# Optimization experiments

Hardware: AMD Instinct MI355X
Metric: run time of the kernel (lower is better)

Reference implementation:

```python
import jax, jax.numpy as jnp
import numpy as np

ALPHA = 1.702
LIMIT = 7.0
TOP_K = 2
B, S, H, E, I = 2, 1024, 768, 8, 768


def setup_inputs() -> dict:
    key = jax.random.key(0)
    ks = jax.random.split(key, 7)
    scale = 0.02
    return {
        "hidden_states": jax.random.normal(ks[0], (B, S, H), dtype=jnp.float32),
        "Wr": jax.random.normal(ks[1], (H, E), dtype=jnp.float32) * scale,
        "br": jax.random.normal(ks[2], (E,), dtype=jnp.float32) * scale,
        "Wgu": jax.random.normal(ks[3], (E, H, 2 * I), dtype=jnp.float32) * scale,
        "bgu": jax.random.normal(ks[4], (E, 2 * I), dtype=jnp.float32) * scale,
        "Wd": jax.random.normal(ks[5], (E, I, H), dtype=jnp.float32) * scale,
        "bd": jax.random.normal(ks[6], (E, H), dtype=jnp.float32) * scale,
    }


def reference(hidden_states, Wr, br, Wgu, bgu, Wd, bd):
    # Router: top-K experts per token, softmax over the K selected logits
    logits = jnp.einsum("bsh,he->bse", hidden_states, Wr) + br
    topk_vals, topk_idx = jax.lax.top_k(logits, TOP_K)        # [B,S,K]
    router_scores = jax.nn.softmax(topk_vals, axis=-1)         # [B,S,K]

    # Dense-over-experts grouped GEMM (sparse_matmul reference: unselected
    # experts are computed but never read by the combine gather below).
    gu = jnp.einsum("bsh,ehf->bsef", hidden_states, Wgu) + bgu  # [B,S,E,2I]
    gu = jnp.minimum(gu, LIMIT)
    gate = gu[..., :I]
    up = jnp.maximum(gu[..., I:], -LIMIT)
    glu = gate * jax.nn.sigmoid(gate * ALPHA)
    activated = (up + 1.0) * glu                                # [B,S,E,I]

    down = jnp.einsum("bsei,eih->bseh", activated, Wd) + bd     # [B,S,E,H]

    # all_to_all_combine (num_devices=1): gather this token's K expert outputs
    sel = jnp.take_along_axis(down, topk_idx[..., None], axis=2)  # [B,S,K,H]
    output = jnp.sum(sel * router_scores[..., None], axis=2)      # [B,S,H]
    return output
```

## Files before the change

kernel.cpp:

```cpp
#include <hip/hip_runtime.h>
#include <hip/hip_bf16.h>
#include <cmath>

#define ALPHA 1.702f
#define LIMIT 7.0f

constexpr int B = 2, S = 1024, H = 768, E = 8, I = 768;
constexpr int T = B * S;
constexpr int TWO_I = 2 * I;
constexpr int CAP = T;
constexpr int NT1 = I / 64;
constexpr int NT2 = H / 64;
constexpr int MT = CAP / 128;

constexpr int RTR_BLKS = 64;
constexpr int WGU_TILES = E * (TWO_I / 64) * (H / 64);
constexpr int WD_TILES  = E * (H / 64) * (H / 64);
constexpr int PRE_BLKS = RTR_BLKS + WGU_TILES;
constexpr int G1_BLKS = MT * E * NT1;
constexpr int K1_BLKS = G1_BLKS + WD_TILES;
constexpr int G2_BLKS = MT * E * NT2;

typedef __attribute__((ext_vector_type(8))) short short8;
typedef __attribute__((ext_vector_type(4))) float floatx4;

__device__ __forceinline__ unsigned short f2bf(float v) {
  __hip_bfloat16 h = __float2bfloat16(v);
  return *reinterpret_cast<unsigned short*>(&h);
}

__device__ __forceinline__ void g2l16(const void* g, void* l) {
  __builtin_amdgcn_global_load_lds(
      (const __attribute__((address_space(1))) void*)g,
      (__attribute__((address_space(3))) void*)l, 16, 0, 0);
}

__device__ __forceinline__ void transpose_tile(
    const float* __restrict__ in, unsigned short* __restrict__ outw,
    int N, int n0, int k0, float (*tile)[65], int tid) {
  constexpr int K = 768;
  int jr = tid & 15, r0 = tid >> 4;
#pragma unroll
  for (int p = 0; p < 4; p++) {
    int k = r0 + p * 16;
    float4 v = *(const float4*)(in + (size_t)(k0 + k) * N + n0 + jr * 4);
    tile[k][jr * 4 + 0] = v.x;
    tile[k][jr * 4 + 1] = v.y;
    tile[k][jr * 4 + 2] = v.z;
    tile[k][jr * 4 + 3] = v.w;
  }
  __syncthreads();
#pragma unroll
  for (int p = 0; p < 4; p++) {
    int n = r0 + p * 16;
    ushort4 o;
    o.x = f2bf(tile[jr * 4 + 0][n]);
    o.y = f2bf(tile[jr * 4 + 1][n]);
    o.z = f2bf(tile[jr * 4 + 2][n]);
    o.w = f2bf(tile[jr * 4 + 3][n]);
    *(ushort4*)(outw + (size_t)(n0 + n) * K + k0 + jr * 4) = o;
  }
}

__global__ __launch_bounds__(256) void pre_router_wgu(
    const float* __restrict__ x, const float* __restrict__ Wr,
    const float* __restrict__ br, const float* __restrict__ Wgu,
    unsigned short* __restrict__ Wgt, unsigned short* __restrict__ xb,
    float* __restrict__ out, int* __restrict__ e_cnt,
    int* __restrict__ row_token, float* __restrict__ row_w) {
  int bid = blockIdx.x;
  int tid = threadIdx.x;

  if (bid < RTR_BLKS) {
    __shared__ int cnt_s[E];
    __shared__ int base_s[E];
    __shared__ int tok_e[E][64];
    __shared__ float wv_e[E][64];

    if (tid < E) cnt_s[tid] = 0;
    __syncthreads();

    int wave = tid >> 6;
    int lane = tid & 63;

    for (int tt = 0; tt < 8; tt++) {
      int t = bid * 32 + wave * 8 + tt;
      const float* xr = x + (size_t)t * H;

      float4 z4 = {0.f, 0.f, 0.f, 0.f};
#pragma unroll
      for (int j = 0; j < 3; j++)
        *(float4*)(out + (size_t)t * H + (size_t)(j * 64 + lane) * 4) = z4;

      float acc[E];
#pragma unroll
      for (int e = 0; e < E; e++) acc[e] = 0.0f;

#pragma unroll
      for (int it = 0; it < 3; it++) {
        int h4 = it * 64 + lane;
        float4 xv = *(const float4*)(xr + (size_t)h4 * 4);
        ushort4 xo;
        xo.x = f2bf(xv.x);
        xo.y = f2bf(xv.y);
        xo.z = f2bf(xv.z);
        xo.w = f2bf(xv.w);
        *(ushort4*)(xb + (size_t)t * H + (size_t)h4 * 4) = xo;
        const float* wrow = Wr + (size_t)h4 * 4 * E;
        float xs[4] = {xv.x, xv.y, xv.z, xv.w};
#pragma unroll
        for (int j = 0; j < 4; j++)
#pragma unroll
          for (int e = 0; e < E; e++) acc[e] += xs[j] * wrow[j * E + e];
      }
#pragma unroll
      for (int e = 0; e < E; e++) {
        float v = acc[e];
        for (int off = 32; off > 0; off >>= 1) v += __shfl_down(v, off, 64);
        acc[e] = v;
      }
      if (lane == 0) {
        float logits[E];
#pragma unroll
        for (int e = 0; e < E; e++) logits[e] = acc[e] + br[e];
        int i0 = 0;
        float v0 = logits[0];
#pragma unroll
        for (int e = 1; e < E; e++)
          if (logits[e] > v0) { v0 = logits[e]; i0 = e; }
        int i1 = -1;
        float v1 = -INFINITY;
#pragma unroll
        for (int e = 0; e < E; e++) {
          if (e == i0) continue;
          if (logits[e] > v1) { v1 = logits[e]; i1 = e; }
        }
        float s1 = __expf(v1 - v0);
        float denom = 1.0f + s1;
        int p0 = atomicAdd(&cnt_s[i0], 1);
        tok_e[i0][p0] = t;
        wv_e[i0][p0] = 1.0f / denom;
        int p1 = atomicAdd(&cnt_s[i1], 1);
        tok_e[i1][p1] = t;
        wv_e[i1][p1] = s1 / denom;
      }
    }
    __syncthreads();
    if (tid < E) base_s[tid] = atomicAdd(&e_cnt[tid], cnt_s[tid]);
    __syncthreads();
#pragma unroll
    for (int e = 0; e < E; e++) {
      int c = cnt_s[e], b0 = base_s[e];
      for (int j = tid; j < c; j += 256) {
        row_token[e * CAP + b0 + j] = tok_e[e][j];
        row_w[e * CAP + b0 + j] = wv_e[e][j];
      }
    }
    return;
  }

  __shared__ float tile[64][65];
  int q = bid - RTR_BLKS;
  int e = q / 288, rem = q % 288;
  int n0 = (rem % 24) * 64;
  int k0 = (rem / 24) * 64;
  transpose_tile(Wgu + (size_t)e * H * TWO_I, Wgt + (size_t)e * TWO_I * H,
                 TWO_I, n0, k0, tile, tid);
}

struct G1Smem {
  short As[2][128 * 64];
  short Bg[2][64 * 64];
  short Bu[2][64 * 64];
  int tok[128];
};
struct TSmem {
  float tile[64][65];
};

__global__ __launch_bounds__(256) void gemm_gu_wdT(
    const unsigned short* __restrict__ xb, const unsigned short* __restrict__ Wgt,
    const float* __restrict__ bgu, const int* __restrict__ e_cnt,
    const int* __restrict__ row_token, unsigned short* __restrict__ act,
    const float* __restrict__ Wd, unsigned short* __restrict__ Wdt) {
  __shared__ __align__(16) char smem_raw[sizeof(G1Smem)];
  int bid = blockIdx.x;
  int tid = threadIdx.x;

  if (bid >= G1_BLKS) {
    TSmem* ts = (TSmem*)smem_raw;
    int q = bid - G1_BLKS;
    int e = q / 144, rem = q % 144;
    int n0 = (rem % 12) * 64;
    int k0 = (rem / 12) * 64;
    transpose_tile(Wd + (size_t)e * H * I, Wdt + (size_t)e * H * I,
                   H, n0, k0, ts->tile, tid);
    return;
  }

  G1Smem* sm = (G1Smem*)smem_raw;
  int g = bid % (E * NT1);
  int mt = bid / (E * NT1);
  int e = g / NT1;
  int n0 = (g % NT1) * 64;
  int cnt = e_cnt[e];
  int m0 = mt * 128;
  if (m0 >= cnt) return;
  int start = e * CAP;
  const unsigned short* Wg = Wgt + (size_t)e * TWO_I * H;
  const float* bias = bgu + (size_t)e * TWO_I;

  if (tid < 128) {
    int m = m0 + tid;
    sm->tok[tid] = row_token[start + ((m < cnt) ? m : (cnt - 1))];
  }
  __syncthreads();

  int lane = tid & 63;
  int wave = tid >> 6;
  int quad = lane >> 4;
  int lrow = lane & 15;
  int wm = (wave >> 1) * 64;
  int wn = (wave & 1) * 32;

  const unsigned short* gA[4];
  int oA[4];
#pragma unroll
  for (int r = 0; r < 4; r++) {
    int s = (wave * 4 + r) * 64 + lane;
    int row = s >> 3;
    int gg = (s & 7) ^ (row & 7);
    gA[r] = xb + (size_t)sm->tok[row] * H + gg * 8;
    oA[r] = (wave * 4 + r) * 64 * 8;
  }
  const unsigned short *gBg[2], *gBu[2];
  int oB[2];
#pragma unroll
  for (int r = 0; r < 2; r++) {
    int s = (wave * 2 + r) * 64 + lane;
    int row = s >> 3;
    int gg = (s & 7) ^ (row & 7);
    gBg[r] = Wg + (size_t)(n0 + row) * H + gg * 8;
    gBu[r] = gBg[r] + (size_t)I * H;
    oB[r] = (wave * 2 + r) * 64 * 8;
  }

  float bgv[2], buv[2];
#pragma unroll
  for (int tj = 0; tj < 2; tj++) {
    int ncol = n0 + wn + tj * 16 + lrow;
    bgv[tj] = bias[ncol];
    buv[tj] = bias[I + ncol];
  }

  floatx4 accg[4][2], accu[4][2];
#pragma unroll
  for (int i = 0; i < 4; i++)
#pragma unroll
    for (int j = 0; j < 2; j++) {
      accg[i][j] = floatx4{0.f, 0.f, 0.f, 0.f};
      accu[i][j] = floatx4{0.f, 0.f, 0.f, 0.f};
    }

  __syncthreads();

#pragma unroll
  for (int r = 0; r < 4; r++) g2l16(gA[r], &sm->As[0][oA[r]]);
#pragma unroll
  for (int r = 0; r < 2; r++) {
    g2l16(gBg[r], &sm->Bg[0][oB[r]]);
    g2l16(gBu[r], &sm->Bu[0][oB[r]]);
  }

  constexpr int NK = H / 64;
  for (int i = 0; i < NK; i++) {
    int cb = i & 1;
    if (i + 1 < NK) {
      int nb = cb ^ 1;
      int k1 = (i + 1) * 64;
#pragma unroll
      for (int r = 0; r < 4; r++) g2l16(gA[r] + k1, &sm->As[nb][oA[r]]);
#pragma unroll
      for (int r = 0; r < 2; r++) {
        g2l16(gBg[r] + k1, &sm->Bg[nb][oB[r]]);
        g2l16(gBu[r] + k1, &sm->Bu[nb][oB[r]]);
      }
      asm volatile("s_waitcnt vmcnt(8)" ::: "memory");
    } else {
      asm volatile("s_waitcnt vmcnt(0)" ::: "memory");
    }
    __builtin_amdgcn_s_barrier();

#pragma unroll
    for (int ks = 0; ks < 2; ks++) {
      int c = ks * 4 + quad;
      short8 a[4], bg[2], bu[2];
#pragma unroll
      for (int ti = 0; ti < 4; ti++) {
        int r = wm + ti * 16 + lrow;
        a[ti] = *(const short8*)(&sm->As[cb][(r * 8 + (c ^ (r & 7))) * 8]);
      }
#pragma unroll
      for (int tj = 0; tj < 2; tj++) {
        int r = wn + tj * 16 + lrow;
        bg[tj] = *(const short8*)(&sm->Bg[cb][(r * 8 + (c ^ (r & 7))) * 8]);
        bu[tj] = *(const short8*)(&sm->Bu[cb][(r * 8 + (c ^ (r & 7))) * 8]);
      }
#pragma unroll
      for (int ti = 0; ti < 4; ti++)
#pragma unroll
        for (int tj = 0; tj < 2; tj++) {
          accg[ti][tj] = __builtin_amdgcn_mfma_f32_16x16x32_bf16(
              a[ti], bg[tj], accg[ti][tj], 0, 0, 0);
          accu[ti][tj] = __builtin_amdgcn_mfma_f32_16x16x32_bf16(
              a[ti], bu[tj], accu[ti][tj], 0, 0, 0);
        }
    }
    __builtin_amdgcn_s_barrier();
  }

#pragma unroll
  for (int ti = 0; ti < 4; ti++) {
#pragma unroll
    for (int tj = 0; tj < 2; tj++) {
      int ncol = n0 + wn + tj * 16 + lrow;
#pragma unroll
      for (int r = 0; r < 4; r++) {
        int m = m0 + wm + ti * 16 + quad * 4 + r;
        if (m < cnt) {
          float gg = accg[ti][tj][r] + bgv[tj];
          float u = accu[ti][tj][r] + buv[tj];
          gg = fminf(gg, LIMIT);
          u = fmaxf(fminf(u, LIMIT), -LIMIT);
          float glu = gg / (1.0f + __expf(-ALPHA * gg));
          act[(size_t)(start + m) * I + ncol] = f2bf((u + 1.0f) * glu);
        }
      }
    }
  }
}

__global__ __launch_bounds__(256) void gemm_down_mfma(
    const unsigned short* __restrict__ act, const unsigned short* __restrict__ Wdt,
    const float* __restrict__ bd, const int* __restrict__ e_cnt,
    const int* __restrict__ row_token, const float* __restrict__ row_w,
    float* __restrict__ out) {
  int bid = blockIdx.x;
  int g = bid % (E * NT2);
  int mt = bid / (E * NT2);
  int e = g / NT2;
  int n0 = (g % NT2) * 64;
  int cnt = e_cnt[e];
  int m0 = mt * 128;
  if (m0 >= cnt) return;
  int start = e * CAP;
  const unsigned short* Wd = Wdt + (size_t)e * H * I;
  const float* bias = bd + (size_t)e * H;

  __shared__ short As[2][128 * 64];
  __shared__ short Bs[2][64 * 64];
  __shared__ int tok[128];
  __shared__ float wts[128];

  int tid = threadIdx.x;
  if (tid < 128) {
    int m = m0 + tid;
    int mm = (m < cnt) ? m : (cnt - 1);
    tok[tid] = row_token[start + mm];
    wts[tid] = row_w[start + mm];
  }
  __syncthreads();

  int lane = tid & 63;
  int wave = tid >> 6;
  int quad = lane >> 4;
  int lrow = lane & 15;
  int wm = (wave >> 1) * 64;
  int wn = (wave & 1) * 32;

  const unsigned short* gA[4];
  int oA[4];
#pragma unroll
  for (int r = 0; r < 4; r++) {
    int s = (wave * 4 + r) * 64 + lane;
    int row = s >> 3;
    int gg = (s & 7) ^ (row & 7);
    int gm = m0 + row;
    int mm = (gm < cnt) ? gm : (cnt - 1);
    gA[r] = act + (size_t)(start + mm) * I + gg * 8;
    oA[r] = (wave * 4 + r) * 64 * 8;
  }
  const unsigned short* gB[2];
  int oB[2];
#pragma unroll
  for (int r = 0; r < 2; r++) {
    int s = (wave * 2 + r) * 64 + lane;
    int row = s >> 3;
    int gg = (s & 7) ^ (row & 7);
    gB[r] = Wd + (size_t)(n0 + row) * I + gg * 8;
    oB[r] = (wave * 2 + r) * 64 * 8;
  }

  float bdv[2];
#pragma unroll
  for (int tj = 0; tj < 2; tj++) bdv[tj] = bias[n0 + wn + tj * 16 + lrow];

  floatx4 acc[4][2];
#pragma unroll
  for (int i = 0; i < 4; i++)
#pragma unroll
    for (int j = 0; j < 2; j++) acc[i][j] = floatx4{0.f, 0.f, 0.f, 0.f};

  __syncthreads();

#pragma unroll
  for (int r = 0; r < 4; r++) g2l16(gA[r], &As[0][oA[r]]);
#pragma unroll
  for (int r = 0; r < 2; r++) g2l16(gB[r], &Bs[0][oB[r]]);

  constexpr int NK = I / 64;
  for (int i = 0; i < NK; i++) {
    int cb = i & 1;
    if (i + 1 < NK) {
      int nb = cb ^ 1;
      int k1 = (i + 1) * 64;
#pragma unroll
      for (int r = 0; r < 4; r++) g2l16(gA[r] + k1, &As[nb][oA[r]]);
#pragma unroll
      for (int r = 0; r < 2; r++) g2l16(gB[r] + k1, &Bs[nb][oB[r]]);
      asm volatile("s_waitcnt vmcnt(6)" ::: "memory");
    } else {
      asm volatile("s_waitcnt vmcnt(0)" ::: "memory");
    }
    __builtin_amdgcn_s_barrier();

#pragma unroll
    for (int ks = 0; ks < 2; ks++) {
      int c = ks * 4 + quad;
      short8 a[4], b[2];
#pragma unroll
      for (int ti = 0; ti < 4; ti++) {
        int r = wm + ti * 16 + lrow;
        a[ti] = *(const short8*)(&As[cb][(r * 8 + (c ^ (r & 7))) * 8]);
      }
#pragma unroll
      for (int tj = 0; tj < 2; tj++) {
        int r = wn + tj * 16 + lrow;
        b[tj] = *(const short8*)(&Bs[cb][(r * 8 + (c ^ (r & 7))) * 8]);
      }
#pragma unroll
      for (int ti = 0; ti < 4; ti++)
#pragma unroll
        for (int tj = 0; tj < 2; tj++)
          acc[ti][tj] = __builtin_amdgcn_mfma_f32_16x16x32_bf16(
              a[ti], b[tj], acc[ti][tj], 0, 0, 0);
    }
    __builtin_amdgcn_s_barrier();
  }

#pragma unroll
  for (int ti = 0; ti < 4; ti++) {
#pragma unroll
    for (int tj = 0; tj < 2; tj++) {
      int ncol = n0 + wn + tj * 16 + lrow;
#pragma unroll
      for (int r = 0; r < 4; r++) {
        int ml = wm + ti * 16 + quad * 4 + r;
        int m = m0 + ml;
        if (m < cnt) {
          atomicAdd(&out[(size_t)tok[ml] * H + ncol],
                    wts[ml] * (acc[ti][tj][r] + bdv[tj]));
        }
      }
    }
  }
}

extern "C" void kernel_launch(void* const* d_in, const int* in_sizes, int n_in,
                              void* d_out, int out_size, void* d_ws,
                              size_t ws_size, hipStream_t stream) {
  const float* x   = (const float*)d_in[0];
  const float* Wr  = (const float*)d_in[1];
  const float* br  = (const float*)d_in[2];
  const float* Wgu = (const float*)d_in[3];
  const float* bgu = (const float*)d_in[4];
  const float* Wd  = (const float*)d_in[5];
  const float* bd  = (const float*)d_in[6];
  float* out = (float*)d_out;

  char* w = (char*)d_ws;
  int* e_cnt = (int*)w;       w += 16 * sizeof(int);
  int* row_token = (int*)w;   w += (size_t)E * CAP * sizeof(int);
  float* row_w = (float*)w;   w += (size_t)E * CAP * sizeof(float);
  unsigned short* xb  = (unsigned short*)w; w += (size_t)T * H * 2;
  unsigned short* Wgt = (unsigned short*)w; w += (size_t)E * TWO_I * H * 2;
  unsigned short* Wdt = (unsigned short*)w; w += (size_t)E * H * I * 2;
  unsigned short* act = (unsigned short*)w; w += (size_t)E * CAP * I * 2;

  hipMemsetAsync(e_cnt, 0, 16 * sizeof(int), stream);
  pre_router_wgu<<<PRE_BLKS, 256, 0, stream>>>(
      x, Wr, br, Wgu, Wgt, xb, out, e_cnt, row_token, row_w);
  gemm_gu_wdT<<<K1_BLKS, 256, 0, stream>>>(
      xb, Wgt, bgu, e_cnt, row_token, act, Wd, Wdt);
  gemm_down_mfma<<<G2_BLKS, 256, 0, stream>>>(
      act, Wdt, bd, e_cnt, row_token, row_w, out);
}
```

Measured before the change: 162.8 us.

## Fuse three MoE kernels into one persistent kernel with grid barriers

```diff
diff --git a/kernel.cpp b/kernel.cpp
--- a/kernel.cpp
+++ b/kernel.cpp
@@ -13,12 +13,14 @@
 constexpr int NT2 = H / 64;
 constexpr int MT = CAP / 128;
 
+constexpr int GRID = 512;
+
 constexpr int RTR_BLKS = 64;
 constexpr int WGU_TILES = E * (TWO_I / 64) * (H / 64);
 constexpr int WD_TILES  = E * (H / 64) * (H / 64);
-constexpr int PRE_BLKS = RTR_BLKS + WGU_TILES;
+constexpr int P0_ITEMS = RTR_BLKS + WGU_TILES;
 constexpr int G1_BLKS = MT * E * NT1;
-constexpr int K1_BLKS = G1_BLKS + WD_TILES;
+constexpr int P1_ITEMS = G1_BLKS + WD_TILES;
 constexpr int G2_BLKS = MT * E * NT2;
 
 typedef __attribute__((ext_vector_type(8))) short short8;
@@ -33,6 +35,45 @@
   __builtin_amdgcn_global_load_lds(
       (const __attribute__((address_space(1))) void*)g,
       (__attribute__((address_space(3))) void*)l, 16, 0, 0);
+}
+
+struct G1Smem {
+  short As[2][128 * 64];
+  short Bg[2][64 * 64];
+  short Bu[2][64 * 64];
+  int tok[128];
+};
+struct G2Smem {
+  short As[2][128 * 64];
+  short Bs[2][64 * 64];
+  int tok[128];
+  float wts[128];
+};
+struct RtrSmem {
+  int cnt_s[E];
+  int base_s[E];
+  int tok_e[E][64];
+  float wv_e[E][64];
+};
+union SmemAll {
+  G1Smem g1;
+  G2Smem g2;
+  float tile[64][65];
+  RtrSmem rtr;
+};
+
+__device__ __forceinline__ void grid_bar(int* cnt, int tid) {
+  __syncthreads();
+  if (tid == 0) {
+    __threadfence();
+    __hip_atomic_fetch_add(cnt, 1, __ATOMIC_ACQ_REL, __HIP_MEMORY_SCOPE_AGENT);
+    while (__hip_atomic_load(cnt, __ATOMIC_ACQUIRE,
+                             __HIP_MEMORY_SCOPE_AGENT) < GRID) {
+      __builtin_amdgcn_s_sleep(2);
+    }
+    __threadfence();
+  }
+  __syncthreads();
 }
 
 __device__ __forceinline__ void transpose_tile(
@@ -62,145 +103,100 @@
   }
 }
 
-__global__ __launch_bounds__(256) void pre_router_wgu(
-    const float* __restrict__ x, const float* __restrict__ Wr,
-    const float* __restrict__ br, const float* __restrict__ Wgu,
-    unsigned short* __restrict__ Wgt, unsigned short* __restrict__ xb,
-    float* __restrict__ out, int* __restrict__ e_cnt,
-    int* __restrict__ row_token, float* __restrict__ row_w) {
-  int bid = blockIdx.x;
-  int tid = threadIdx.x;
-
-  if (bid < RTR_BLKS) {
-    __shared__ int cnt_s[E];
-    __shared__ int base_s[E];
-    __shared__ int tok_e[E][64];
-    __shared__ float wv_e[E][64];
-
-    if (tid < E) cnt_s[tid] = 0;
-    __syncthreads();
-
-    int wave = tid >> 6;
-    int lane = tid & 63;
-
-    for (int tt = 0; tt < 8; tt++) {
-      int t = bid * 32 + wave * 8 + tt;
-      const float* xr = x + (size_t)t * H;
-
-      float4 z4 = {0.f, 0.f, 0.f, 0.f};
-#pragma unroll
-      for (int j = 0; j < 3; j++)
-        *(float4*)(out + (size_t)t * H + (size_t)(j * 64 + lane) * 4) = z4;
-
-      float acc[E];
-#pragma unroll
-      for (int e = 0; e < E; e++) acc[e] = 0.0f;
-
-#pragma unroll
-      for (int it = 0; it < 3; it++) {
-        int h4 = it * 64 + lane;
-        float4 xv = *(const float4*)(xr + (size_t)h4 * 4);
-        ushort4 xo;
-        xo.x = f2bf(xv.x);
-        xo.y = f2bf(xv.y);
-        xo.z = f2bf(xv.z);
-        xo.w = f2bf(xv.w);
-        *(ushort4*)(xb + (size_t)t * H + (size_t)h4 * 4) = xo;
-        const float* wrow = Wr + (size_t)h4 * 4 * E;
-        float xs[4] = {xv.x, xv.y, xv.z, xv.w};
-#pragma unroll
-        for (int j = 0; j < 4; j++)
-#pragma unroll
-          for (int e = 0; e < E; e++) acc[e] += xs[j] * wrow[j * E + e];
-      }
+__device__ __forceinline__ void router_item(
+    int rbid, int tid, RtrSmem& rs, const float* __restrict__ x,
+    const float* __restrict__ Wr, const float* __restrict__ br,
+    unsigned short* __restrict__ xb, float* __restrict__ out,
+    int* __restrict__ e_cnt, int* __restrict__ row_token,
+    float* __restrict__ row_w) {
+  if (tid < E) rs.cnt_s[tid] = 0;
+  __syncthreads();
+
+  int wave = tid >> 6;
+  int lane = tid & 63;
+
+  for (int tt = 0; tt < 8; tt++) {
+    int t = rbid * 32 + wave * 8 + tt;
+    const float* xr = x + (size_t)t * H;
+
+    float4 z4 = {0.f, 0.f, 0.f, 0.f};
+#pragma unroll
+    for (int j = 0; j < 3; j++)
+      *(float4*)(out + (size_t)t * H + (size_t)(j * 64 + lane) * 4) = z4;
+
+    float acc[E];
+#pragma unroll
+    for (int e = 0; e < E; e++) acc[e] = 0.0f;
+
+#pragma unroll
+    for (int it = 0; it < 3; it++) {
+      int h4 = it * 64 + lane;
+      float4 xv = *(const float4*)(xr + (size_t)h4 * 4);
+      ushort4 xo;
+      xo.x = f2bf(xv.x);
+      xo.y = f2bf(xv.y);
+      xo.z = f2bf(xv.z);
+      xo.w = f2bf(xv.w);
+      *(ushort4*)(xb + (size_t)t * H + (size_t)h4 * 4) = xo;
+      const float* wrow = Wr + (size_t)h4 * 4 * E;
+      float xs[4] = {xv.x, xv.y, xv.z, xv.w};
+#pragma unroll
+      for (int j = 0; j < 4; j++)
+#pragma unroll
+        for (int e = 0; e < E; e++) acc[e] += xs[j] * wrow[j * E + e];
+    }
+#pragma unroll
+    for (int e = 0; e < E; e++) {
+      float v = acc[e];
+      for (int off = 32; off > 0; off >>= 1) v += __shfl_down(v, off, 64);
+      acc[e] = v;
+    }
+    if (lane == 0) {
+      float logits[E];
+#pragma unroll
+      for (int e = 0; e < E; e++) logits[e] = acc[e] + br[e];
+      int i0 = 0;
+      float v0 = logits[0];
+#pragma unroll
+      for (int e = 1; e < E; e++)
+        if (logits[e] > v0) { v0 = logits[e]; i0 = e; }
+      int i1 = -1;
+      float v1 = -INFINITY;
 #pragma unroll
       for (int e = 0; e < E; e++) {
-        float v = acc[e];
-        for (int off = 32; off > 0; off >>= 1) v += __shfl_down(v, off, 64);
-        acc[e] = v;
-      }
-      if (lane == 0) {
-        float logits[E];
-#pragma unroll
-        for (int e = 0; e < E; e++) logits[e] = acc[e] + br[e];
-        int i0 = 0;
-        float v0 = logits[0];
-#pragma unroll
-        for (int e = 1; e < E; e++)
-          if (logits[e] > v0) { v0 = logits[e]; i0 = e; }
-        int i1 = -1;
-        float v1 = -INFINITY;
-#pragma unroll
-        for (int e = 0; e < E; e++) {
-          if (e == i0) continue;
-          if (logits[e] > v1) { v1 = logits[e]; i1 = e; }
-        }
-        float s1 = __expf(v1 - v0);
-        float denom = 1.0f + s1;
-        int p0 = atomicAdd(&cnt_s[i0], 1);
-        tok_e[i0][p0] = t;
-        wv_e[i0][p0] = 1.0f / denom;
-        int p1 = atomicAdd(&cnt_s[i1], 1);
-        tok_e[i1][p1] = t;
-        wv_e[i1][p1] = s1 / denom;
-      }
-    }
-    __syncthreads();
-    if (tid < E) base_s[tid] = atomicAdd(&e_cnt[tid], cnt_s[tid]);
-    __syncthreads();
-#pragma unroll
-    for (int e = 0; e < E; e++) {
-      int c = cnt_s[e], b0 = base_s[e];
-      for (int j = tid; j < c; j += 256) {
-        row_token[e * CAP + b0 + j] = tok_e[e][j];
-        row_w[e * CAP + b0 + j] = wv_e[e][j];
-      }
-    }
-    return;
-  }
-
-  __shared__ float tile[64][65];
-  int q = bid - RTR_BLKS;
-  int e = q / 288, rem = q % 288;
-  int n0 = (rem % 24) * 64;
-  int k0 = (rem / 24) * 64;
-  transpose_tile(Wgu + (size_t)e * H * TWO_I, Wgt + (size_t)e * TWO_I * H,
-                 TWO_I, n0, k0, tile, tid);
-}
-
-struct G1Smem {
-  short As[2][128 * 64];
-  short Bg[2][64 * 64];
-  short Bu[2][64 * 64];
-  int tok[128];
-};
-struct TSmem {
-  float tile[64][65];
-};
-
-__global__ __launch_bounds__(256) void gemm_gu_wdT(
-    const unsigned short* __restrict__ xb, const unsigned short* __restrict__ Wgt,
-    const float* __restrict__ bgu, const int* __restrict__ e_cnt,
-    const int* __restrict__ row_token, unsigned short* __restrict__ act,
-    const float* __restrict__ Wd, unsigned short* __restrict__ Wdt) {
-  __shared__ __align__(16) char smem_raw[sizeof(G1Smem)];
-  int bid = blockIdx.x;
-  int tid = threadIdx.x;
-
-  if (bid >= G1_BLKS) {
-    TSmem* ts = (TSmem*)smem_raw;
-    int q = bid - G1_BLKS;
-    int e = q / 144, rem = q % 144;
-    int n0 = (rem % 12) * 64;
-    int k0 = (rem / 12) * 64;
-    transpose_tile(Wd + (size_t)e * H * I, Wdt + (size_t)e * H * I,
-                   H, n0, k0, ts->tile, tid);
-    return;
-  }
-
-  G1Smem* sm = (G1Smem*)smem_raw;
-  int g = bid % (E * NT1);
-  int mt = bid / (E * NT1);
+        if (e == i0) continue;
+        if (logits[e] > v1) { v1 = logits[e]; i1 = e; }
+      }
+      float s1 = __expf(v1 - v0);
+      float denom = 1.0f + s1;
+      int p0 = atomicAdd(&rs.cnt_s[i0], 1);
+      rs.tok_e[i0][p0] = t;
+      rs.wv_e[i0][p0] = 1.0f / denom;
+      int p1 = atomicAdd(&rs.cnt_s[i1], 1);
+      rs.tok_e[i1][p1] = t;
+      rs.wv_e[i1][p1] = s1 / denom;
+    }
+  }
+  __syncthreads();
+  if (tid < E) rs.base_s[tid] = atomicAdd(&e_cnt[tid], rs.cnt_s[tid]);
+  __syncthreads();
+#pragma unroll
+  for (int e = 0; e < E; e++) {
+    int c = rs.cnt_s[e], b0 = rs.base_s[e];
+    for (int j = tid; j < c; j += 256) {
+      row_token[e * CAP + b0 + j] = rs.tok_e[e][j];
+      row_w[e * CAP + b0 + j] = rs.wv_e[e][j];
+    }
+  }
+}
+
+__device__ __forceinline__ void gemm1_item(
+    int item, int tid, G1Smem& sm, const unsigned short* __restrict__ xb,
+    const unsigned short* __restrict__ Wgt, const float* __restrict__ bgu,
+    const int* __restrict__ e_cnt, const int* __restrict__ row_token,
+    unsigned short* __restrict__ act) {
+  int g = item % (E * NT1);
+  int mt = item / (E * NT1);
   int e = g / NT1;
   int n0 = (g % NT1) * 64;
   int cnt = e_cnt[e];
@@ -212,7 +208,7 @@
 
   if (tid < 128) {
     int m = m0 + tid;
-    sm->tok[tid] = row_token[start + ((m < cnt) ? m : (cnt - 1))];
+    sm.tok[tid] = row_token[start + ((m < cnt) ? m : (cnt - 1))];
   }
   __syncthreads();
 
@@ -230,7 +226,7 @@
     int s = (wave * 4 + r) * 64 + lane;
     int row = s >> 3;
     int gg = (s & 7) ^ (row & 7);
-    gA[r] = xb + (size_t)sm->tok[row] * H + gg * 8;
+    gA[r] = xb + (size_t)sm.tok[row] * H + gg * 8;
     oA[r] = (wave * 4 + r) * 64 * 8;
   }
   const unsigned short *gBg[2], *gBu[2];
@@ -265,11 +261,11 @@
   __syncthreads();
 
 #pragma unroll
-  for (int r = 0; r < 4; r++) g2l16(gA[r], &sm->As[0][oA[r]]);
+  for (int r = 0; r < 4; r++) g2l16(gA[r], &sm.As[0][oA[r]]);
 #pragma unroll
   for (int r = 0; r < 2; r++) {
-    g2l16(gBg[r], &sm->Bg[0][oB[r]]);
-    g2l16(gBu[r], &sm->Bu[0][oB[r]]);
+    g2l16(gBg[r], &sm.Bg[0][oB[r]]);
+    g2l16(gBu[r], &sm.Bu[0][oB[r]]);
   }
 
   constexpr int NK = H / 64;
@@ -279,11 +275,11 @@
       int nb = cb ^ 1;
       int k1 = (i + 1) * 64;
 #pragma unroll
-      for (int r = 0; r < 4; r++) g2l16(gA[r] + k1, &sm->As[nb][oA[r]]);
+      for (int r = 0; r < 4; r++) g2l16(gA[r] + k1, &sm.As[nb][oA[r]]);
 #pragma unroll
       for (int r = 0; r < 2; r++) {
-        g2l16(gBg[r] + k1, &sm->Bg[nb][oB[r]]);
-        g2l16(gBu[r] + k1, &sm->Bu[nb][oB[r]]);
+        g2l16(gBg[r] + k1, &sm.Bg[nb][oB[r]]);
+        g2l16(gBu[r] + k1, &sm.Bu[nb][oB[r]]);
       }
       asm volatile("s_waitcnt vmcnt(8)" ::: "memory");
     } else {
@@ -298,13 +294,13 @@
 #pragma unroll
       for (int ti = 0; ti < 4; ti++) {
         int r = wm + ti * 16 + lrow;
-        a[ti] = *(const short8*)(&sm->As[cb][(r * 8 + (c ^ (r & 7))) * 8]);
+        a[ti] = *(const short8*)(&sm.As[cb][(r * 8 + (c ^ (r & 7))) * 8]);
       }
 #pragma unroll
       for (int tj = 0; tj < 2; tj++) {
         int r = wn + tj * 16 + lrow;
-        bg[tj] = *(const short8*)(&sm->Bg[cb][(r * 8 + (c ^ (r & 7))) * 8]);
-        bu[tj] = *(const short8*)(&sm->Bu[cb][(r * 8 + (c ^ (r & 7))) * 8]);
+        bg[tj] = *(const short8*)(&sm.Bg[cb][(r * 8 + (c ^ (r & 7))) * 8]);
+        bu[tj] = *(const short8*)(&sm.Bu[cb][(r * 8 + (c ^ (r & 7))) * 8]);
       }
 #pragma unroll
       for (int ti = 0; ti < 4; ti++)
@@ -340,14 +336,13 @@
   }
 }
 
-__global__ __launch_bounds__(256) void gemm_down_mfma(
-    const unsigned short* __restrict__ act, const unsigned short* __restrict__ Wdt,
-    const float* __restrict__ bd, const int* __restrict__ e_cnt,
-    const int* __restrict__ row_token, const float* __restrict__ row_w,
-    float* __restrict__ out) {
-  int bid = blockIdx.x;
-  int g = bid % (E * NT2);
-  int mt = bid / (E * NT2);
+__device__ __forceinline__ void gemm2_item(
+    int item, int tid, G2Smem& sm, const unsigned short* __restrict__ act,
+    const unsigned short* __restrict__ Wdt, const float* __restrict__ bd,
+    const int* __restrict__ e_cnt, const int* __restrict__ row_token,
+    const float* __restrict__ row_w, float* __restrict__ out) {
+  int g = item % (E * NT2);
+  int mt = item / (E * NT2);
   int e = g / NT2;
   int n0 = (g % NT2) * 64;
   int cnt = e_cnt[e];
@@ -357,17 +352,11 @@
   const unsigned short* Wd = Wdt + (size_t)e * H * I;
   const float* bias = bd + (size_t)e * H;
 
-  __shared__ short As[2][128 * 64];
-  __shared__ short Bs[2][64 * 64];
-  __shared__ int tok[128];
-  __shared__ float wts[128];
-
-  int tid = threadIdx.x;
   if (tid < 128) {
     int m = m0 + tid;
     int mm = (m < cnt) ? m : (cnt - 1);
-    tok[tid] = row_token[start + mm];
-    wts[tid] = row_w[start + mm];
+    sm.tok[tid] = row_token[start + mm];
+    sm.wts[tid] = row_w[start + mm];
   }
   __syncthreads();
 
@@ -414,9 +403,9 @@
   __syncthreads();
 
 #pragma unroll
-  for (int r = 0; r < 4; r++) g2l16(gA[r], &As[0][oA[r]]);
-#pragma unroll
-  for (int r = 0; r < 2; r++) g2l16(gB[r], &Bs[0][oB[r]]);
+  for (int r = 0; r < 4; r++) g2l16(gA[r], &sm.As[0][oA[r]]);
+#pragma unroll
+  for (int r = 0; r < 2; r++) g2l16(gB[r], &sm.Bs[0][oB[r]]);
 
   constexpr int NK = I / 64;
   for (int i = 0; i < NK; i++) {
@@ -425,9 +414,9 @@
       int nb = cb ^ 1;
       int k1 = (i + 1) * 64;
 #pragma unroll
-      for (int r = 0; r < 4; r++) g2l16(gA[r] + k1, &As[nb][oA[r]]);
-#pragma unroll
-      for (int r = 0; r < 2; r++) g2l16(gB[r] + k1, &Bs[nb][oB[r]]);
+      for (int r = 0; r < 4; r++) g2l16(gA[r] + k1, &sm.As[nb][oA[r]]);
+#pragma unroll
+      for (int r = 0; r < 2; r++) g2l16(gB[r] + k1, &sm.Bs[nb][oB[r]]);
       asm volatile("s_waitcnt vmcnt(6)" ::: "memory");
     } else {
       asm volatile("s_waitcnt vmcnt(0)" ::: "memory");
@@ -441,12 +430,12 @@
 #pragma unroll
       for (int ti = 0; ti < 4; ti++) {
         int r = wm + ti * 16 + lrow;
-        a[ti] = *(const short8*)(&As[cb][(r * 8 + (c ^ (r & 7))) * 8]);
+        a[ti] = *(const short8*)(&sm.As[cb][(r * 8 + (c ^ (r & 7))) * 8]);
       }
 #pragma unroll
       for (int tj = 0; tj < 2; tj++) {
         int r = wn + tj * 16 + lrow;
-        b[tj] = *(const short8*)(&Bs[cb][(r * 8 + (c ^ (r & 7))) * 8]);
+        b[tj] = *(const short8*)(&sm.Bs[cb][(r * 8 + (c ^ (r & 7))) * 8]);
       }
 #pragma unroll
       for (int ti = 0; ti < 4; ti++)
@@ -468,11 +457,66 @@
         int ml = wm + ti * 16 + quad * 4 + r;
         int m = m0 + ml;
         if (m < cnt) {
-          atomicAdd(&out[(size_t)tok[ml] * H + ncol],
-                    wts[ml] * (acc[ti][tj][r] + bdv[tj]));
+          atomicAdd(&out[(size_t)sm.tok[ml] * H + ncol],
+                    sm.wts[ml] * (acc[ti][tj][r] + bdv[tj]));
         }
       }
     }
+  }
+}
+
+__global__ __launch_bounds__(256, 2) void fused_all(
+    const float* __restrict__ x, const float* __restrict__ Wr,
+    const float* __restrict__ br, const float* __restrict__ Wgu,
+    const float* __restrict__ Wd, const float* __restrict__ bgu,
+    const float* __restrict__ bd, unsigned short* __restrict__ Wgt,
+    unsigned short* __restrict__ Wdt, unsigned short* __restrict__ xb,
+    unsigned short* __restrict__ act, float* __restrict__ out,
+    int* __restrict__ e_cnt, int* __restrict__ row_token,
+    float* __restrict__ row_w, int* __restrict__ bar) {
+  __shared__ __align__(16) SmemAll sm;
+  int tid = threadIdx.x;
+  int bid = blockIdx.x;
+
+  for (int i = bid; i < P0_ITEMS; i += GRID) {
+    __syncthreads();
+    int c = i >> 3, o = i & 7;
+    int g = c / 37, r = c % 37;
+    if (r == 0) {
+      router_item(g * 8 + o, tid, sm.rtr, x, Wr, br, xb, out, e_cnt,
+                  row_token, row_w);
+    } else {
+      int q = (g * 36 + (r - 1)) * 8 + o;
+      int e = q / 288, rem = q % 288;
+      int n0 = (rem % 24) * 64;
+      int k0 = (rem / 24) * 64;
+      transpose_tile(Wgu + (size_t)e * H * TWO_I, Wgt + (size_t)e * TWO_I * H,
+                     TWO_I, n0, k0, sm.tile, tid);
+    }
+  }
+  grid_bar(&bar[0], tid);
+
+  for (int i = bid; i < P1_ITEMS; i += GRID) {
+    __syncthreads();
+    int c = i >> 3, o = i & 7;
+    int g = c / 7, r = c % 7;
+    if (r < 4) {
+      gemm1_item((g * 4 + r) * 8 + o, tid, sm.g1, xb, Wgt, bgu, e_cnt,
+                 row_token, act);
+    } else {
+      int q = (g * 3 + (r - 4)) * 8 + o;
+      int e = q / 144, rem = q % 144;
+      int n0 = (rem % 12) * 64;
+      int k0 = (rem / 12) * 64;
+      transpose_tile(Wd + (size_t)e * H * I, Wdt + (size_t)e * H * I, H, n0,
+                     k0, sm.tile, tid);
+    }
+  }
+  grid_bar(&bar[1], tid);
+
+  for (int i = bid; i < G2_BLKS; i += GRID) {
+    __syncthreads();
+    gemm2_item(i, tid, sm.g2, act, Wdt, bd, e_cnt, row_token, row_w, out);
   }
 }
 
@@ -490,6 +534,7 @@
 
   char* w = (char*)d_ws;
   int* e_cnt = (int*)w;       w += 16 * sizeof(int);
+  int* bar = e_cnt + 8;
   int* row_token = (int*)w;   w += (size_t)E * CAP * sizeof(int);
   float* row_w = (float*)w;   w += (size_t)E * CAP * sizeof(float);
   unsigned short* xb  = (unsigned short*)w; w += (size_t)T * H * 2;
@@ -498,10 +543,7 @@
   unsigned short* act = (unsigned short*)w; w += (size_t)E * CAP * I * 2;
 
   hipMemsetAsync(e_cnt, 0, 16 * sizeof(int), stream);
-  pre_router_wgu<<<PRE_BLKS, 256, 0, stream>>>(
-      x, Wr, br, Wgu, Wgt, xb, out, e_cnt, row_token, row_w);
-  gemm_gu_wdT<<<K1_BLKS, 256, 0, stream>>>(
-      xb, Wgt, bgu, e_cnt, row_token, act, Wd, Wdt);
-  gemm_down_mfma<<<G2_BLKS, 256, 0, stream>>>(
-      act, Wdt, bd, e_cnt, row_token, row_w, out);
-}
+  fused_all<<<GRID, 256, 0, stream>>>(
+      x, Wr, br, Wgu, Wd, bgu, bd, Wgt, Wdt, xb, act, out, e_cnt, row_token,
+      row_w, bar);
+}
```

New measurement: 547.1 us. 236% more time.
